# Optimization experiments

Hardware: AMD Instinct MI355X
Metric: run time of the kernel (lower is better)

The kernel has to match this reference:

```python
import jax, jax.numpy as jnp
import numpy as np

N_HEAD = 8


def setup_inputs() -> dict:
    key = jax.random.key(0)
    ks = jax.random.split(key, 8)
    v, b, c, h, w = 8, 4, 512, 16, 16
    s = 1.0 / np.sqrt(c).astype(np.float32)
    return {
        "q": jax.random.normal(ks[0], (v, b, c, h, w), jnp.float32),
        "kv": jax.random.normal(ks[1], (v, b, c, h, w), jnp.float32),
        "Wq": jax.random.normal(ks[2], (c, c), jnp.float32) * s,
        "bq": jnp.zeros((c,), jnp.float32),
        "Wkv": jax.random.normal(ks[3], (c, 2 * c), jnp.float32) * s,
        "bkv": jnp.zeros((2 * c,), jnp.float32),
        "Wp": jax.random.normal(ks[4], (c, c), jnp.float32) * s,
        "bp": jnp.zeros((c,), jnp.float32),
    }


def reference(q, kv, Wq, bq, Wkv, bkv, Wp, bp):
    vi, bi, ci, hi, wi = q.shape
    hw = hi * wi
    T = vi * hw
    hd = ci // N_HEAD

    # rearrange 'v b c h w -> b (v h w) c'
    xq = q.transpose(1, 0, 3, 4, 2).reshape(bi, T, ci)
    xkv = kv.transpose(1, 0, 3, 4, 2).reshape(bi, T, ci)

    qp = xq @ Wq + bq                      # [b, T, c]
    k, v_ = jnp.split(xkv @ Wkv + bkv, 2, axis=-1)

    def heads(x):
        return x.reshape(bi, T, N_HEAD, hd).transpose(0, 2, 1, 3)  # [b,h,T,d]

    qh, kh, vh = heads(qp), heads(k), heads(v_)

    att = jnp.einsum('bhqd,bhkd->bhqk', qh, kh) * (1.0 / np.sqrt(hd).astype(np.float32))

    # block-causal mask: query block (size h*w) may attend to key blocks <= its own
    blocks = jnp.arange(T) // hw
    mask = blocks[:, None] >= blocks[None, :]
    att = jnp.where(mask, att, -jnp.inf)
    att = jax.nn.softmax(att, axis=-1)

    y = jnp.einsum('bhqk,bhkd->bhqd', att, vh)
    y = y.transpose(0, 2, 1, 3).reshape(bi, T, ci)
    y = y @ Wp + bp

    # rearrange 'b (v h w) c -> v b c h w'
    return y.reshape(bi, vi, hi, wi, ci).transpose(1, 0, 4, 2, 3)
```

## Files before the change

### kernel.cpp

```cpp
#include <hip/hip_runtime.h>
#include <hip/hip_bf16.h>
#include <cmath>

typedef unsigned short u16;
typedef __attribute__((ext_vector_type(8))) short s8v;
typedef __attribute__((ext_vector_type(4))) float f4v;
typedef __attribute__((ext_vector_type(2))) float f2v;
typedef __attribute__((ext_vector_type(4))) unsigned int u32x4;
typedef __attribute__((ext_vector_type(4))) unsigned short u16x4;

#define MFMA(a,b,c) __builtin_amdgcn_mfma_f32_16x16x32_bf16((a),(b),(c),0,0,0)

__device__ __forceinline__ float bf2f(u16 u) {
    union { float f; unsigned i; } x; x.i = ((unsigned)u) << 16; return x.f;
}
__device__ __forceinline__ u16 f2bf(float f) {
    union { float f; unsigned i; } x; x.f = f;
    unsigned r = x.i + 0x7FFFu + ((x.i >> 16) & 1u);
    return (u16)(r >> 16);
}
__device__ __forceinline__ unsigned cvtpk(float lo, float hi) {
    unsigned r;
    asm("v_cvt_pk_bf16_f32 %0, %1, %2" : "=v"(r) : "v"(lo), "v"(hi));
    return r;
}
__device__ __forceinline__ void gload_lds16(const void* g, void* l) {
    __builtin_amdgcn_global_load_lds(
        (const __attribute__((address_space(1))) unsigned int*)g,
        (__attribute__((address_space(3))) unsigned int*)l, 16, 0, 0);
}
__device__ __forceinline__ int swb(int row, int colb) {
    return row * 128 + (colb ^ ((((row >> 4) ^ row) & 7) << 4));
}

__constant__ int CPER[8]  = {1,1,2,2,3,3,4,4};
__constant__ int POFF[17] = {0,1,2,3,4,6,8,10,12,15,18,21,24,28,32,36,40};

__global__ __launch_bounds__(256)
void qkv_proj(const float* __restrict__ q, const float* __restrict__ kv,
              const float* __restrict__ Wq, const float* __restrict__ bq,
              const float* __restrict__ Wkv, const float* __restrict__ bkv,
              u16* __restrict__ QH, u16* __restrict__ KH, u16* __restrict__ VT)
{
    __shared__ __align__(16) u16 Al[128 * 64];
    __shared__ __align__(16) u16 Bl[128 * 64];

    const int bid = blockIdx.x;
    const int x = bid & 7, i = bid >> 3;
    const int mt = x + 8 * (i / 12);
    const int nt = i % 12;
    const int m0 = mt << 7, n0 = nt << 7;

    const int tid  = threadIdx.x;
    const int lane = tid & 63;
    const int w    = tid >> 6;
    const int wr = (w >> 1) * 64, wc = (w & 1) * 64;
    const int cl = lane & 15, rl = lane >> 4;

    const int bb  = m0 >> 11;
    const int t0  = m0 & 2047;
    const int vv  = t0 >> 8;
    const int hw0 = t0 & 255;

    const float* Abase = ((nt < 4) ? q : kv) + (size_t)(vv * 4 + bb) * 131072 + hw0;

    const float* W; const float* bias; int NW, wn0, dn0; u16* dst;
    if (nt < 4)      { W = Wq;  bias = bq;  NW = 512;  wn0 = n0;       dn0 = n0;        dst = QH; }
    else if (nt < 8) { W = Wkv; bias = bkv; NW = 1024; wn0 = n0 - 512; dn0 = n0 - 512;  dst = KH; }
    else             { W = Wkv; bias = bkv; NW = 1024; wn0 = n0 - 512; dn0 = n0 - 1024; dst = VT; }

    const float oscale = (nt < 4) ? 0.18033688011f : 1.0f;

    f4v acc[4][4] = {};
    f2v la[8], lb[8];

    const int mh = tid & 63;
    const int kb = tid >> 6;

#define QKV_LOAD(k0_) do {                                                   \
        const float* gA = Abase + (size_t)((k0_) + kb * 8) * 256 + mh * 2;   \
        const float* gB = W + (size_t)((k0_) + kb * 8) * NW + wn0 + mh * 2;  \
        _Pragma("unroll")                                                    \
        for (int j = 0; j < 8; ++j) {                                        \
            la[j] = *reinterpret_cast<const f2v*>(gA + j * 256);             \
            lb[j] = *reinterpret_cast<const f2v*>(gB + (size_t)j * NW);      \
        }                                                                    \
    } while (0)

    QKV_LOAD(0);

    for (int k0 = 0; k0 < 512; k0 += 32) {
        #pragma unroll
        for (int e = 0; e < 2; ++e) {
            u32x4 pa, pb;
            #pragma unroll
            for (int jj = 0; jj < 4; ++jj) {
                pa[jj] = cvtpk(la[jj * 2][e], la[jj * 2 + 1][e]);
                pb[jj] = cvtpk(lb[jj * 2][e], lb[jj * 2 + 1][e]);
            }
            *(u32x4*)((char*)Al + swb(mh * 2 + e, kb * 16)) = pa;
            *(u32x4*)((char*)Bl + swb(mh * 2 + e, kb * 16)) = pb;
        }
        __syncthreads();
        if (k0 + 32 < 512) QKV_LOAD(k0 + 32);

        s8v af[4], bf[4];
        #pragma unroll
        for (int mi = 0; mi < 4; ++mi)
            af[mi] = *(const s8v*)((const char*)Al + swb(wr + mi * 16 + cl, rl * 16));
        #pragma unroll
        for (int ni = 0; ni < 4; ++ni)
            bf[ni] = *(const s8v*)((const char*)Bl + swb(wc + ni * 16 + cl, rl * 16));
        #pragma unroll
        for (int mi = 0; mi < 4; ++mi)
            #pragma unroll
            for (int ni = 0; ni < 4; ++ni)
                acc[mi][ni] = MFMA(af[mi], bf[ni], acc[mi][ni]);
        __syncthreads();
    }
#undef QKV_LOAD

    if (nt < 8) {
        #pragma unroll
        for (int ni = 0; ni < 4; ++ni) {
            const int nl   = wc + ni * 16 + cl;
            const float bv = bias[wn0 + nl];
            const int cout = dn0 + nl;
            const int hh = cout >> 6, dd = cout & 63;
            const size_t obase = ((size_t)(bb * 8 + hh) * 2048) * 64 + dd;
            #pragma unroll
            for (int mi = 0; mi < 4; ++mi)
                #pragma unroll
                for (int r = 0; r < 4; ++r) {
                    const int m = m0 + wr + mi * 16 + rl * 4 + r;
                    const int t = m & 2047;
                    dst[obase + (size_t)t * 64] = f2bf((acc[mi][ni][r] + bv) * oscale);
                }
        }
    } else {
        #pragma unroll
        for (int ni = 0; ni < 4; ++ni) {
            const int nl   = wc + ni * 16 + cl;
            const float bv = bias[wn0 + nl];
            const int cout = dn0 + nl;
            const int hh = cout >> 6, dd = cout & 63;
            const size_t obase = ((size_t)(bb * 8 + hh) * 64 + dd) * 2048;
            #pragma unroll
            for (int mi = 0; mi < 4; ++mi) {
                const int m = m0 + wr + mi * 16 + rl * 4;
                const int t = m & 2047;
                u16x4 pk;
                #pragma unroll
                for (int r = 0; r < 4; ++r) pk[r] = f2bf(acc[mi][ni][r] + bv);
                *reinterpret_cast<u16x4*>(dst + obase + t) = pk;
            }
        }
    }
}

__global__ __launch_bounds__(256, 3)
void attn_part(const u16* __restrict__ QH, const u16* __restrict__ KH,
               const u16* __restrict__ VT,
               u16* __restrict__ Opart, float* __restrict__ ML)
{
    __shared__ __align__(16) u16 Kl[2][4096];
    __shared__ __align__(16) u16 Vl[2][4096];
    __shared__ u16 Pl[4][32][36];

    const int wg = blockIdx.x;
    const int bh = wg & 31;
    const int s  = 39 - (wg >> 5);
    int p = 0;
    #pragma unroll
    for (int i = 0; i < 15; ++i) p += (s >= POFF[i + 1]) ? 1 : 0;
    const int c  = s - POFF[p];
    const int qb = p >> 1;
    const int kstart = c * 512;
    const int nk = min(512, (qb + 1) * 256 - kstart);
    const int nt64 = nk >> 6;

    const int tid = threadIdx.x, lane = tid & 63, w = tid >> 6;
    const int cl = lane & 15, rl = lane >> 4;

    const u16* Qb = QH + (size_t)bh * 131072;
    const u16* Kb = KH + (size_t)bh * 131072;
    const u16* Vb = VT + (size_t)bh * 131072;

    const int qrow0 = p * 128 + w * 32;

    s8v qf[2][2];
    #pragma unroll
    for (int mi = 0; mi < 2; ++mi)
        #pragma unroll
        for (int kf = 0; kf < 2; ++kf)
            qf[mi][kf] = *reinterpret_cast<const s8v*>(
                Qb + (size_t)(qrow0 + mi * 16 + cl) * 64 + kf * 32 + rl * 8);

    unsigned kofs[2], vofs[2];
    #pragma unroll
    for (int i = 0; i < 2; ++i) {
        const int f = w * 128 + i * 64 + lane;
        const int row = f >> 3;
        kofs[i] = row * 128 + (((f & 7) * 16) ^ ((row & 7) << 4));
        vofs[i] = row * 4096 + (((f & 7) * 16) ^ ((row & 7) << 4));
    }

#define ISSUE(bufi, kb0_) do {                                               \
        const char* kG = (const char*)Kb + (size_t)(kb0_) * 128;             \
        const char* vG = (const char*)Vb + (size_t)(kb0_) * 2;               \
        char* kL = (char*)&Kl[bufi][0] + w * 2048;                           \
        char* vL = (char*)&Vl[bufi][0] + w * 2048;                           \
        _Pragma("unroll")                                                    \
        for (int i_ = 0; i_ < 2; ++i_) {                                     \
            gload_lds16(kG + kofs[i_], kL + i_ * 1024);                      \
            gload_lds16(vG + vofs[i_], vL + i_ * 1024);                      \
        }                                                                    \
    } while (0)

    f4v o[2][4] = {};
    float lp[8] = {0.f, 0.f, 0.f, 0.f, 0.f, 0.f, 0.f, 0.f};

    ISSUE(0, kstart);

    for (int kt = 0; kt < nt64; ++kt) {
        asm volatile("s_waitcnt vmcnt(0)" ::: "memory");
        __builtin_amdgcn_sched_barrier(0);
        __syncthreads();
        if (kt + 1 < nt64) ISSUE((kt + 1) & 1, kstart + (kt + 1) * 64);

        const char* Kbase = (const char*)&Kl[kt & 1][0];
        const char* Vbase = (const char*)&Vl[kt & 1][0];

        f4v sc[2][4] = {};
        #pragma unroll
        for (int ni = 0; ni < 4; ++ni)
            #pragma unroll
            for (int kf = 0; kf < 2; ++kf) {
                const int row = ni * 16 + cl;
                s8v kfr = *reinterpret_cast<const s8v*>(
                    Kbase + row * 128 + ((kf * 64 + rl * 16) ^ ((row & 7) << 4)));
                sc[0][ni] = MFMA(qf[0][kf], kfr, sc[0][ni]);
                sc[1][ni] = MFMA(qf[1][kf], kfr, sc[1][ni]);
            }

        #pragma unroll
        for (int mi = 0; mi < 2; ++mi)
            #pragma unroll
            for (int ni = 0; ni < 4; ++ni)
                #pragma unroll
                for (int r = 0; r < 4; ++r)
                    sc[mi][ni][r] = exp2f(sc[mi][ni][r]);
        #pragma unroll
        for (int mi = 0; mi < 2; ++mi)
            #pragma unroll
            for (int r = 0; r < 4; ++r)
                lp[mi * 4 + r] += sc[mi][0][r] + sc[mi][1][r]
                                + sc[mi][2][r] + sc[mi][3][r];

        #pragma unroll
        for (int kw = 0; kw < 2; ++kw) {
            #pragma unroll
            for (int mi = 0; mi < 2; ++mi)
                #pragma unroll
                for (int jj = 0; jj < 2; ++jj) {
                    const int ni = kw * 2 + jj;
                    const unsigned w0 = cvtpk(sc[mi][ni][0], sc[mi][ni][1]);
                    const unsigned w1 = cvtpk(sc[mi][ni][2], sc[mi][ni][3]);
                    const int col = jj * 16 + cl;
                    Pl[w][mi * 16 + rl * 4 + 0][col] = (u16)w0;
                    Pl[w][mi * 16 + rl * 4 + 1][col] = (u16)(w0 >> 16);
                    Pl[w][mi * 16 + rl * 4 + 2][col] = (u16)w1;
                    Pl[w][mi * 16 + rl * 4 + 3][col] = (u16)(w1 >> 16);
                }
            s8v pf0 = *reinterpret_cast<const s8v*>(&Pl[w][cl][rl * 8]);
            s8v pf1 = *reinterpret_cast<const s8v*>(&Pl[w][16 + cl][rl * 8]);
            #pragma unroll
            for (int di = 0; di < 4; ++di) {
                const int row = di * 16 + cl;
                s8v vf = *reinterpret_cast<const s8v*>(
                    Vbase + row * 128 + ((kw * 64 + rl * 16) ^ ((row & 7) << 4)));
                o[0][di] = MFMA(pf0, vf, o[0][di]);
                o[1][di] = MFMA(pf1, vf, o[1][di]);
            }
        }
    }
#undef ISSUE

    const int slot = bh * 40 + POFF[p] + c;
    #pragma unroll
    for (int mi = 0; mi < 2; ++mi)
        #pragma unroll
        for (int r = 0; r < 4; ++r) {
            const int idx = mi * 4 + r;
            float ls = lp[idx];
            ls += __shfl_xor(ls, 1);
            ls += __shfl_xor(ls, 2);
            ls += __shfl_xor(ls, 4);
            ls += __shfl_xor(ls, 8);
            const float inv = 1.f / ls;
            const int rloc = w * 32 + mi * 16 + rl * 4 + r;
            if (cl == 0) ML[(size_t)slot * 128 + rloc] = ls;
            #pragma unroll
            for (int di = 0; di < 4; ++di)
                Opart[(size_t)slot * 8192 + rloc * 64 + di * 16 + cl] =
                    f2bf(o[mi][di][r] * inv);
        }
}

__global__ __launch_bounds__(256)
void attn_combine(const u16* __restrict__ Opart, const float* __restrict__ ML,
                  u16* __restrict__ YH)
{
    const int wg = blockIdx.x;
    const int bh = wg & 31;
    const int p  = wg >> 5;
    const int b = bh >> 3, h = bh & 7;
    const int nc = CPER[p >> 1];
    const int sb = bh * 40 + POFF[p];

    const int t = threadIdx.x;
    const int rloc = t >> 1;
    const int dh = (t & 1) * 32;

    float lc[4], L = 0.f;
    for (int c = 0; c < nc; ++c) {
        lc[c] = ML[(size_t)(sb + c) * 128 + rloc];
        L += lc[c];
    }
    const float invL = 1.f / L;
    float wgt[4];
    for (int c = 0; c < nc; ++c) wgt[c] = lc[c] * invL;

    f4v a[8] = {};
    for (int c = 0; c < nc; ++c) {
        const float wv = wgt[c];
        #pragma unroll
        for (int u = 0; u < 4; ++u) {
            s8v vv = *reinterpret_cast<const s8v*>(
                &Opart[(size_t)(sb + c) * 8192 + rloc * 64 + dh + u * 8]);
            #pragma unroll
            for (int e = 0; e < 4; ++e) a[u * 2][e]     += wv * bf2f((u16)vv[e]);
            #pragma unroll
            for (int e = 0; e < 4; ++e) a[u * 2 + 1][e] += wv * bf2f((u16)vv[e + 4]);
        }
    }

    const size_t ybase = ((size_t)b * 2048 + p * 128 + rloc) * 512 + h * 64 + dh;
    #pragma unroll
    for (int u = 0; u < 4; ++u) {
        s8v ov;
        #pragma unroll
        for (int e = 0; e < 4; ++e) ov[e]     = (short)f2bf(a[u * 2][e]);
        #pragma unroll
        for (int e = 0; e < 4; ++e) ov[e + 4] = (short)f2bf(a[u * 2 + 1][e]);
        *reinterpret_cast<s8v*>(YH + ybase + u * 8) = ov;
    }
}

__global__ __launch_bounds__(256)
void out_proj(const u16* __restrict__ YH, const float* __restrict__ Wp,
              const float* __restrict__ bp, float* __restrict__ out)
{
    __shared__ __align__(16) u16 Al[128 * 64];
    __shared__ u16 Bl[128][40];

    const int bid = blockIdx.x;
    const int x = bid & 7, i = bid >> 3;
    const int mt = x + 8 * (i >> 2);
    const int ct = i & 3;
    const int c0 = ct << 7, m0 = mt << 7;

    const int tid = threadIdx.x, lane = tid & 63, w = tid >> 6;
    const int wr = (w >> 1) * 64, wc = (w & 1) * 64;
    const int cl = lane & 15, rl = lane >> 4;

    f4v acc[4][4] = {};
    f2v wa[8];
    s8v sy[2];

    const int mh = tid & 63;
    const int kb = tid >> 6;
    const int br = tid >> 2;
    const int bq4 = (tid & 3) * 8;

#define OP_LOAD(k0_) do {                                                    \
        const float* gA = Wp + (size_t)((k0_) + kb * 8) * 512 + c0 + mh * 2; \
        _Pragma("unroll")                                                    \
        for (int j = 0; j < 8; ++j)                                          \
            wa[j] = *reinterpret_cast<const f2v*>(gA + j * 512);             \
        _Pragma("unroll")                                                    \
        for (int it = 0; it < 2; ++it)                                       \
            sy[it] = *reinterpret_cast<const s8v*>(                          \
                YH + (size_t)(m0 + br + it * 64) * 512 + (k0_) + bq4);       \
    } while (0)

    OP_LOAD(0);

    for (int k0 = 0; k0 < 512; k0 += 32) {
        #pragma unroll
        for (int e = 0; e < 2; ++e) {
            u32x4 pa;
            #pragma unroll
            for (int jj = 0; jj < 4; ++jj)
                pa[jj] = cvtpk(wa[jj * 2][e], wa[jj * 2 + 1][e]);
            *(u32x4*)((char*)Al + swb(mh * 2 + e, kb * 16)) = pa;
        }
        #pragma unroll
        for (int it = 0; it < 2; ++it)
            *reinterpret_cast<s8v*>(&Bl[br + it * 64][bq4]) = sy[it];
        __syncthreads();
        if (k0 + 32 < 512) OP_LOAD(k0 + 32);

        s8v af[4], bfr[4];
        #pragma unroll
        for (int mi = 0; mi < 4; ++mi)
            af[mi] = *(const s8v*)((const char*)Al + swb(wr + mi * 16 + cl, rl * 16));
        #pragma unroll
        for (int ni = 0; ni < 4; ++ni)
            bfr[ni] = *reinterpret_cast<const s8v*>(&Bl[wc + ni * 16 + cl][rl * 8]);
        #pragma unroll
        for (int mi = 0; mi < 4; ++mi)
            #pragma unroll
            for (int ni = 0; ni < 4; ++ni)
                acc[mi][ni] = MFMA(af[mi], bfr[ni], acc[mi][ni]);
        __syncthreads();
    }
#undef OP_LOAD

    #pragma unroll
    for (int mi = 0; mi < 4; ++mi)
        #pragma unroll
        for (int r = 0; r < 4; ++r) {
            const int c = c0 + wr + mi * 16 + rl * 4 + r;
            const float bv = bp[c];
            #pragma unroll
            for (int ni = 0; ni < 4; ++ni) {
                const int tok = m0 + wc + ni * 16 + cl;
                const int bb = tok >> 11, t = tok & 2047;
                const int vv = t >> 8, hw = t & 255;
                out[(size_t)(vv * 4 + bb) * 131072 + (size_t)c * 256 + hw] =
                    acc[mi][ni][r] + bv;
            }
        }
}

extern "C" void kernel_launch(void* const* d_in, const int* in_sizes, int n_in,
                              void* d_out, int out_size, void* d_ws, size_t ws_size,
                              hipStream_t stream)
{
    const float* q   = (const float*)d_in[0];
    const float* kv  = (const float*)d_in[1];
    const float* Wq  = (const float*)d_in[2];
    const float* bq  = (const float*)d_in[3];
    const float* Wkv = (const float*)d_in[4];
    const float* bkv = (const float*)d_in[5];
    const float* Wp  = (const float*)d_in[6];
    const float* bp  = (const float*)d_in[7];
    float* out = (float*)d_out;

    u16* ws = (u16*)d_ws;
    u16* QH = ws;
    u16* KH = QH + 4194304;
    u16* VT = KH + 4194304;
    u16* YH = VT + 4194304;
    u16* Opart = YH + 4194304;
    float* ML  = (float*)(Opart + 10485760);

    hipLaunchKernelGGL(qkv_proj, dim3(768), dim3(256), 0, stream,
                       q, kv, Wq, bq, Wkv, bkv, QH, KH, VT);
    hipLaunchKernelGGL(attn_part, dim3(1280), dim3(256), 0, stream,
                       QH, KH, VT, Opart, ML);
    hipLaunchKernelGGL(attn_combine, dim3(512), dim3(256), 0, stream,
                       Opart, ML, YH);
    hipLaunchKernelGGL(out_proj, dim3(256), dim3(256), 0, stream, YH, Wp, bp, out);
}
```

Before: 110.8 us.

## Double-buffer LDS tiles in QKV and output projection GEMMs

Both projection GEMMs now use two LDS buffers and two register staging sets. The loop is unrolled by two so the next tile can be converted and written to LDS and the one after that fetched from global memory, all while MFMAs run on the current buffer. This halves the number of barriers per k-step and overlaps LDS writes with compute. In exchange it doubles LDS use and raises register pressure, which may lower occupancy.

```diff
diff --git a/kernel.cpp b/kernel.cpp
--- a/kernel.cpp
+++ b/kernel.cpp
@@ -42,8 +42,8 @@
               const float* __restrict__ Wkv, const float* __restrict__ bkv,
               u16* __restrict__ QH, u16* __restrict__ KH, u16* __restrict__ VT)
 {
-    __shared__ __align__(16) u16 Al[128 * 64];
-    __shared__ __align__(16) u16 Bl[128 * 64];
+    __shared__ __align__(16) u16 Al[2][128 * 64];
+    __shared__ __align__(16) u16 Bl[2][128 * 64];
 
     const int bid = blockIdx.x;
     const int x = bid & 7, i = bid >> 3;
@@ -72,53 +72,72 @@
     const float oscale = (nt < 4) ? 0.18033688011f : 1.0f;
 
     f4v acc[4][4] = {};
-    f2v la[8], lb[8];
+    f2v la0[8], lb0[8], la1[8], lb1[8];
 
     const int mh = tid & 63;
     const int kb = tid >> 6;
 
-#define QKV_LOAD(k0_) do {                                                   \
+#define QKV_LOAD(dA, dB, k0_) do {                                           \
         const float* gA = Abase + (size_t)((k0_) + kb * 8) * 256 + mh * 2;   \
         const float* gB = W + (size_t)((k0_) + kb * 8) * NW + wn0 + mh * 2;  \
         _Pragma("unroll")                                                    \
         for (int j = 0; j < 8; ++j) {                                        \
-            la[j] = *reinterpret_cast<const f2v*>(gA + j * 256);             \
-            lb[j] = *reinterpret_cast<const f2v*>(gB + (size_t)j * NW);      \
+            dA[j] = *reinterpret_cast<const f2v*>(gA + j * 256);             \
+            dB[j] = *reinterpret_cast<const f2v*>(gB + (size_t)j * NW);      \
         }                                                                    \
     } while (0)
 
-    QKV_LOAD(0);
-
-    for (int k0 = 0; k0 < 512; k0 += 32) {
-        #pragma unroll
-        for (int e = 0; e < 2; ++e) {
-            u32x4 pa, pb;
-            #pragma unroll
-            for (int jj = 0; jj < 4; ++jj) {
-                pa[jj] = cvtpk(la[jj * 2][e], la[jj * 2 + 1][e]);
-                pb[jj] = cvtpk(lb[jj * 2][e], lb[jj * 2 + 1][e]);
-            }
-            *(u32x4*)((char*)Al + swb(mh * 2 + e, kb * 16)) = pa;
-            *(u32x4*)((char*)Bl + swb(mh * 2 + e, kb * 16)) = pb;
-        }
+#define QKV_WRITE(bufi, sA, sB) do {                                         \
+        _Pragma("unroll")                                                    \
+        for (int e = 0; e < 2; ++e) {                                        \
+            u32x4 pa, pb;                                                    \
+            _Pragma("unroll")                                                \
+            for (int jj = 0; jj < 4; ++jj) {                                 \
+                pa[jj] = cvtpk(sA[jj * 2][e], sA[jj * 2 + 1][e]);            \
+                pb[jj] = cvtpk(sB[jj * 2][e], sB[jj * 2 + 1][e]);            \
+            }                                                                \
+            *(u32x4*)((char*)&Al[bufi][0] + swb(mh * 2 + e, kb * 16)) = pa;  \
+            *(u32x4*)((char*)&Bl[bufi][0] + swb(mh * 2 + e, kb * 16)) = pb;  \
+        }                                                                    \
+    } while (0)
+
+#define QKV_MFMA(bufi) do {                                                  \
+        s8v af[4], bf[4];                                                    \
+        _Pragma("unroll")                                                    \
+        for (int mi = 0; mi < 4; ++mi)                                       \
+            af[mi] = *(const s8v*)((const char*)&Al[bufi][0]                 \
+                                   + swb(wr + mi * 16 + cl, rl * 16));       \
+        _Pragma("unroll")                                                    \
+        for (int ni = 0; ni < 4; ++ni)                                       \
+            bf[ni] = *(const s8v*)((const char*)&Bl[bufi][0]                 \
+                                   + swb(wc + ni * 16 + cl, rl * 16));       \
+        _Pragma("unroll")                                                    \
+        for (int mi = 0; mi < 4; ++mi)                                       \
+            _Pragma("unroll")                                                \
+            for (int ni = 0; ni < 4; ++ni)                                   \
+                acc[mi][ni] = MFMA(af[mi], bf[ni], acc[mi][ni]);             \
+    } while (0)
+
+    QKV_LOAD(la0, lb0, 0);
+    QKV_WRITE(0, la0, lb0);
+    QKV_LOAD(la1, lb1, 32);
+    __syncthreads();
+
+    #pragma unroll
+    for (int it = 0; it < 8; ++it) {
+        const int t = it * 2;
+        QKV_WRITE(1, la1, lb1);
+        if (t + 2 < 16) QKV_LOAD(la0, lb0, (t + 2) * 32);
+        QKV_MFMA(0);
         __syncthreads();
-        if (k0 + 32 < 512) QKV_LOAD(k0 + 32);
-
-        s8v af[4], bf[4];
-        #pragma unroll
-        for (int mi = 0; mi < 4; ++mi)
-            af[mi] = *(const s8v*)((const char*)Al + swb(wr + mi * 16 + cl, rl * 16));
-        #pragma unroll
-        for (int ni = 0; ni < 4; ++ni)
-            bf[ni] = *(const s8v*)((const char*)Bl + swb(wc + ni * 16 + cl, rl * 16));
-        #pragma unroll
-        for (int mi = 0; mi < 4; ++mi)
-            #pragma unroll
-            for (int ni = 0; ni < 4; ++ni)
-                acc[mi][ni] = MFMA(af[mi], bf[ni], acc[mi][ni]);
+        if (t + 2 < 16) QKV_WRITE(0, la0, lb0);
+        if (t + 3 < 16) QKV_LOAD(la1, lb1, (t + 3) * 32);
+        QKV_MFMA(1);
         __syncthreads();
     }
 #undef QKV_LOAD
+#undef QKV_WRITE
+#undef QKV_MFMA
 
     if (nt < 8) {
         #pragma unroll
@@ -361,8 +380,8 @@
 void out_proj(const u16* __restrict__ YH, const float* __restrict__ Wp,
               const float* __restrict__ bp, float* __restrict__ out)
 {
-    __shared__ __align__(16) u16 Al[128 * 64];
-    __shared__ u16 Bl[128][40];
+    __shared__ __align__(16) u16 Al[2][128 * 64];
+    __shared__ u16 Bl[2][128][40];
 
     const int bid = blockIdx.x;
     const int x = bid & 7, i = bid >> 3;
@@ -375,57 +394,76 @@
     const int cl = lane & 15, rl = lane >> 4;
 
     f4v acc[4][4] = {};
-    f2v wa[8];
-    s8v sy[2];
+    f2v wa0[8], wa1[8];
+    s8v sy0[2], sy1[2];
 
     const int mh = tid & 63;
     const int kb = tid >> 6;
     const int br = tid >> 2;
     const int bq4 = (tid & 3) * 8;
 
-#define OP_LOAD(k0_) do {                                                    \
+#define OP_LOAD(dA, dY, k0_) do {                                            \
         const float* gA = Wp + (size_t)((k0_) + kb * 8) * 512 + c0 + mh * 2; \
         _Pragma("unroll")                                                    \
         for (int j = 0; j < 8; ++j)                                          \
-            wa[j] = *reinterpret_cast<const f2v*>(gA + j * 512);             \
+            dA[j] = *reinterpret_cast<const f2v*>(gA + j * 512);             \
         _Pragma("unroll")                                                    \
         for (int it = 0; it < 2; ++it)                                       \
-            sy[it] = *reinterpret_cast<const s8v*>(                          \
+            dY[it] = *reinterpret_cast<const s8v*>(                          \
                 YH + (size_t)(m0 + br + it * 64) * 512 + (k0_) + bq4);       \
     } while (0)
 
-    OP_LOAD(0);
-
-    for (int k0 = 0; k0 < 512; k0 += 32) {
-        #pragma unroll
-        for (int e = 0; e < 2; ++e) {
-            u32x4 pa;
-            #pragma unroll
-            for (int jj = 0; jj < 4; ++jj)
-                pa[jj] = cvtpk(wa[jj * 2][e], wa[jj * 2 + 1][e]);
-            *(u32x4*)((char*)Al + swb(mh * 2 + e, kb * 16)) = pa;
-        }
-        #pragma unroll
-        for (int it = 0; it < 2; ++it)
-            *reinterpret_cast<s8v*>(&Bl[br + it * 64][bq4]) = sy[it];
+#define OP_WRITE(bufi, sA, sY) do {                                          \
+        _Pragma("unroll")                                                    \
+        for (int e = 0; e < 2; ++e) {                                        \
+            u32x4 pa;                                                        \
+            _Pragma("unroll")                                                \
+            for (int jj = 0; jj < 4; ++jj)                                   \
+                pa[jj] = cvtpk(sA[jj * 2][e], sA[jj * 2 + 1][e]);            \
+            *(u32x4*)((char*)&Al[bufi][0] + swb(mh * 2 + e, kb * 16)) = pa;  \
+        }                                                                    \
+        _Pragma("unroll")                                                    \
+        for (int it = 0; it < 2; ++it)                                       \
+            *reinterpret_cast<s8v*>(&Bl[bufi][br + it * 64][bq4]) = sY[it];  \
+    } while (0)
+
+#define OP_MFMA(bufi) do {                                                   \
+        s8v af[4], bfr[4];                                                   \
+        _Pragma("unroll")                                                    \
+        for (int mi = 0; mi < 4; ++mi)                                       \
+            af[mi] = *(const s8v*)((const char*)&Al[bufi][0]                 \
+                                   + swb(wr + mi * 16 + cl, rl * 16));       \
+        _Pragma("unroll")                                                    \
+        for (int ni = 0; ni < 4; ++ni)                                       \
+            bfr[ni] = *reinterpret_cast<const s8v*>(                         \
+                &Bl[bufi][wc + ni * 16 + cl][rl * 8]);                       \
+        _Pragma("unroll")                                                    \
+        for (int mi = 0; mi < 4; ++mi)                                       \
+            _Pragma("unroll")                                                \
+            for (int ni = 0; ni < 4; ++ni)                                   \
+                acc[mi][ni] = MFMA(af[mi], bfr[ni], acc[mi][ni]);            \
+    } while (0)
+
+    OP_LOAD(wa0, sy0, 0);
+    OP_WRITE(0, wa0, sy0);
+    OP_LOAD(wa1, sy1, 32);
+    __syncthreads();
+
+    #pragma unroll
+    for (int it = 0; it < 8; ++it) {
+        const int t = it * 2;
+        OP_WRITE(1, wa1, sy1);
+        if (t + 2 < 16) OP_LOAD(wa0, sy0, (t + 2) * 32);
+        OP_MFMA(0);
         __syncthreads();
-        if (k0 + 32 < 512) OP_LOAD(k0 + 32);
-
-        s8v af[4], bfr[4];
-        #pragma unroll
-        for (int mi = 0; mi < 4; ++mi)
-            af[mi] = *(const s8v*)((const char*)Al + swb(wr + mi * 16 + cl, rl * 16));
-        #pragma unroll
-        for (int ni = 0; ni < 4; ++ni)
-            bfr[ni] = *reinterpret_cast<const s8v*>(&Bl[wc + ni * 16 + cl][rl * 8]);
-        #pragma unroll
-        for (int mi = 0; mi < 4; ++mi)
-            #pragma unroll
-            for (int ni = 0; ni < 4; ++ni)
-                acc[mi][ni] = MFMA(af[mi], bfr[ni], acc[mi][ni]);
+        if (t + 2 < 16) OP_WRITE(0, wa0, sy0);
+        if (t + 3 < 16) OP_LOAD(wa1, sy1, (t + 3) * 32);
+        OP_MFMA(1);
         __syncthreads();
     }
 #undef OP_LOAD
+#undef OP_WRITE
+#undef OP_MFMA
 
     #pragma unroll
     for (int mi = 0; mi < 4; ++mi)
```

Result: faster. 107.2 us (-3.2%).
